# Kernel tuning notes

Measured on AMD Instinct MI355X. Metric: run time of the kernel, lower is better.

The kernel has to match this reference:

```python
import jax, jax.numpy as jnp
import numpy as np

B, S, NI, NQK, NV = 8, 2048, 1024, 128, 128

def setup_inputs() -> dict:
    key = jax.random.key(0)
    ks = jax.random.split(key, 7)
    sc_i = 1.0 / np.sqrt(NI)
    x = jax.random.normal(ks[0], (B, S, NI), dtype=jnp.float32)
    Wq = jax.random.uniform(ks[1], (NQK, NI), dtype=jnp.float32, minval=-sc_i, maxval=sc_i)
    bq = jax.random.uniform(ks[2], (NQK,), dtype=jnp.float32, minval=-sc_i, maxval=sc_i)
    Wk = jax.random.uniform(ks[3], (NQK, NI), dtype=jnp.float32, minval=-sc_i, maxval=sc_i)
    bk = jax.random.uniform(ks[4], (NQK,), dtype=jnp.float32, minval=-sc_i, maxval=sc_i)
    Wv = jax.random.uniform(ks[5], (NV, NI), dtype=jnp.float32, minval=-sc_i, maxval=sc_i)
    bv = jax.random.uniform(ks[6], (NV,), dtype=jnp.float32, minval=-sc_i, maxval=sc_i)
    return {"x": x, "Wq": Wq, "bq": bq, "Wk": Wk, "bk": bk, "Wv": Wv, "bv": bv}

def reference(x, Wq, bq, Wk, bk, Wv, bv):
    # torch nn.Linear: y = x @ W.T + b
    q = jnp.einsum('bsi,di->bsd', x, Wq) + bq  # [B,S,NQK]
    k = jnp.einsum('bsi,di->bsd', x, Wk) + bk  # [B,S,NQK]
    v = jnp.einsum('bsi,di->bsd', x, Wv) + bv  # [B,S,NV]
    # NOTE: original has no 1/sqrt(d) scaling
    Z = jnp.einsum('bqd,bkd->bqk', q, k)       # [B,S,S]
    Z = jax.nn.softmax(Z, axis=2)
    y = jnp.einsum('bqk,bkd->bqd', Z, v)       # [B,S,NV]
    return y
```

## Files before the change

kernel.cpp:

```cpp
#include <hip/hip_runtime.h>
#include <hip/hip_bf16.h>
#include <cstdint>

#define B_ 8
#define S_ 2048
#define NI_ 1024
#define D_ 128
#define M_ (B_ * S_)

typedef __attribute__((ext_vector_type(8))) short bf16x8;
typedef __attribute__((ext_vector_type(8))) unsigned short u16x8;
typedef __attribute__((ext_vector_type(4))) float f32x4;

__device__ __forceinline__ unsigned short f2bf(float f) {
    union { float f; uint32_t u; } v; v.f = f;
    uint32_t u = v.u;
    u += 0x7fff + ((u >> 16) & 1);
    return (unsigned short)(u >> 16);
}

__device__ __forceinline__ void gload16(const void* g, void* l) {
    __builtin_amdgcn_global_load_lds((const __attribute__((address_space(1))) void*)g,
                                     (__attribute__((address_space(3))) void*)l, 16, 0, 0);
}

__global__ __launch_bounds__(256) void k_cvt_x(const float* __restrict__ x,
                                               unsigned short* __restrict__ xb) {
    int t = blockIdx.x * 256 + threadIdx.x;
    long base = (long)t * 8;
    float4 a = *(const float4*)(x + base);
    float4 b = *(const float4*)(x + base + 4);
    u16x8 r;
    r[0] = f2bf(a.x); r[1] = f2bf(a.y); r[2] = f2bf(a.z); r[3] = f2bf(a.w);
    r[4] = f2bf(b.x); r[5] = f2bf(b.y); r[6] = f2bf(b.z); r[7] = f2bf(b.w);
    *(u16x8*)(xb + base) = r;
}

__global__ __launch_bounds__(256) void k_pack_w(const float* __restrict__ Wq, const float* __restrict__ bq,
                                                const float* __restrict__ Wk, const float* __restrict__ bk,
                                                const float* __restrict__ Wv, const float* __restrict__ bv,
                                                unsigned short* __restrict__ wb, float* __restrict__ bias) {
    int t = blockIdx.x * 256 + threadIdx.x;
    int e = t * 8;
    const float* src; int off;
    if (e < 131072)      { src = Wq; off = e; }
    else if (e < 262144) { src = Wk; off = e - 131072; }
    else                 { src = Wv; off = e - 262144; }
    float4 a = *(const float4*)(src + off);
    float4 b = *(const float4*)(src + off + 4);
    u16x8 r;
    r[0] = f2bf(a.x); r[1] = f2bf(a.y); r[2] = f2bf(a.z); r[3] = f2bf(a.w);
    r[4] = f2bf(b.x); r[5] = f2bf(b.y); r[6] = f2bf(b.z); r[7] = f2bf(b.w);
    *(u16x8*)(wb + e) = r;
    if (t < 384)
        bias[t] = (t < 128) ? bq[t] : (t < 256) ? bk[t - 128] : bv[t - 256];
}

__global__ __launch_bounds__(256) void k_qkv(const unsigned short* __restrict__ xb,
                                             const unsigned short* __restrict__ wb,
                                             const float* __restrict__ bias,
                                             unsigned short* __restrict__ q,
                                             unsigned short* __restrict__ kout,
                                             unsigned short* __restrict__ vT) {
    __shared__ __align__(16) unsigned short As[2][64 * 64];
    __shared__ __align__(16) unsigned short Bs[2][128 * 64];
    const int tid = threadIdx.x;
    const int m0 = blockIdx.x * 64;
    const int n0 = blockIdx.y * 128;
    const int l = tid & 63, w = tid >> 6;
    const int wr = w >> 1, wc = w & 1;
    const int lr = l & 15, lg = l >> 4;
    const int lsw = (lr & 7) << 4;

    const int srow = tid >> 3;
    const int scol = ((tid & 7) * 8) ^ (((tid >> 3) & 7) << 3);

#define GLOADA(buf, k0off) do { \
    _Pragma("unroll") \
    for (int c = 0; c < 2; c++) \
        gload16(xb + (long)(m0 + c * 32 + srow) * NI_ + (k0off) + scol, \
                (unsigned short*)As[buf] + c * 2048 + tid * 8); } while (0)

#define GLOADB(buf, k0off) do { \
    _Pragma("unroll") \
    for (int c = 0; c < 4; c++) \
        gload16(wb + (long)(n0 + c * 32 + srow) * NI_ + (k0off) + scol, \
                (unsigned short*)Bs[buf] + c * 2048 + tid * 8); } while (0)

    f32x4 acc[2][4] = {};

    GLOADA(0, 0);
    GLOADB(0, 0);
    __syncthreads();

    int cur = 0;
    for (int k0 = 0; k0 < NI_; k0 += 64) {
        bool more = (k0 + 64 < NI_);
        if (more) {
            GLOADA(cur ^ 1, k0 + 64);
            GLOADB(cur ^ 1, k0 + 64);
        }

        const char* ad = (const char*)As[cur];
        const char* bd = (const char*)Bs[cur];
        bf16x8 a[2][2], b[4][2];
#pragma unroll
        for (int i = 0; i < 2; i++)
#pragma unroll
            for (int kc = 0; kc < 2; kc++)
                a[i][kc] = *(const bf16x8*)(ad + (wr * 32 + i * 16 + lr) * 128
                                               + ((kc * 64 + lg * 16) ^ lsw));
#pragma unroll
        for (int j = 0; j < 4; j++)
#pragma unroll
            for (int kc = 0; kc < 2; kc++)
                b[j][kc] = *(const bf16x8*)(bd + (wc * 64 + j * 16 + lr) * 128
                                               + ((kc * 64 + lg * 16) ^ lsw));
#pragma unroll
        for (int kc = 0; kc < 2; kc++)
#pragma unroll
            for (int i = 0; i < 2; i++)
#pragma unroll
                for (int j = 0; j < 4; j++)
                    acc[i][j] = __builtin_amdgcn_mfma_f32_16x16x32_bf16(a[i][kc], b[j][kc], acc[i][j], 0, 0, 0);

        __syncthreads();
        cur ^= 1;
    }
#undef GLOADA
#undef GLOADB

#pragma unroll
    for (int i = 0; i < 2; i++)
#pragma unroll
        for (int j = 0; j < 4; j++)
#pragma unroll
            for (int r = 0; r < 4; r++) {
                int row = m0 + wr * 32 + i * 16 + lg * 4 + r;
                int n = n0 + wc * 64 + j * 16 + lr;
                float val = acc[i][j][r] + bias[n];
                unsigned short bv16 = f2bf(val);
                if (n0 == 0)        q[(long)row * 128 + n] = bv16;
                else if (n0 == 128) kout[(long)row * 128 + (n - 128)] = bv16;
                else {
                    int bb = row >> 11, s = row & 2047, d = n - 256;
                    vT[((long)bb * 128 + d) * (long)S_ + s] = bv16;
                }
            }
}

#define SHIFT_ 16.0f
__global__ __launch_bounds__(256, 2) void k_attn(const unsigned short* __restrict__ q,
                                                 const unsigned short* __restrict__ kk,
                                                 const unsigned short* __restrict__ vT,
                                                 float* __restrict__ o_part,
                                                 float* __restrict__ L_part) {
    __shared__ __align__(16) unsigned short Kl[2 * 64 * 128];
    __shared__ __align__(16) unsigned short Vl[2 * 128 * 64];
    __shared__ __align__(16) unsigned short Plds[4 * 32 * 64];
    const int tid = threadIdx.x, l = tid & 63, w = tid >> 6;
    const int b = blockIdx.z, ks = blockIdx.y;
    const int q0 = blockIdx.x * 128 + w * 32;
    const int lr = l & 15, lg = l >> 4;
    const unsigned short* qB = q  + (long)b * S_ * 128;
    const unsigned short* kB = kk + (long)b * S_ * 128;
    const unsigned short* vB = vT + (long)b * 128 * S_;
    char* Pw = (char*)Plds + w * 4096;
    const int kv_base = ks * 512;
    const int lsw = (lr & 7) << 4;

    const int krowc = tid >> 4;
    const int ksrc  = ((tid & 15) * 8) ^ (((tid >> 4) & 7) << 3);
    const int vrowc = tid >> 3;
    const int vsrc  = ((tid & 7) * 8) ^ (((tid >> 3) & 7) << 3);

#define STAGEKV(buf, kvoff) do { \
    unsigned short* kdst = (unsigned short*)Kl + (buf) * 8192; \
    unsigned short* vdst = (unsigned short*)Vl + (buf) * 8192; \
    _Pragma("unroll") \
    for (int c = 0; c < 4; c++) { \
        gload16(kB + (long)((kvoff) + c * 16 + krowc) * 128 + ksrc, kdst + c * 2048 + tid * 8); \
        gload16(vB + (long)(c * 32 + vrowc) * S_ + (kvoff) + vsrc,  vdst + c * 2048 + tid * 8); \
    } } while (0)

    bf16x8 qf[2][4];
#pragma unroll
    for (int a = 0; a < 2; a++)
#pragma unroll
        for (int kc = 0; kc < 4; kc++)
            qf[a][kc] = *(const bf16x8*)(qB + (long)(q0 + a * 16 + lr) * 128 + kc * 32 + lg * 8);

    STAGEKV(0, kv_base);
    __syncthreads();

    float psum[2][4] = {};
    f32x4 o[2][8] = {};
    int cur = 0;

    for (int t = 0; t < 8; t++) {
        if (t < 7) STAGEKV(cur ^ 1, kv_base + (t + 1) * 64);

        const char* kd = (const char*)Kl + cur * 16384;
        const char* vd = (const char*)Vl + cur * 16384;

        f32x4 sa[2][4] = {};
#pragma unroll
        for (int j = 0; j < 4; j++) {
            bf16x8 kf[4];
#pragma unroll
            for (int kc = 0; kc < 4; kc++)
                kf[kc] = *(const bf16x8*)(kd + (((j * 16 + lr) * 256 + kc * 64 + lg * 16) ^ lsw));
#pragma unroll
            for (int a = 0; a < 2; a++)
#pragma unroll
                for (int kc = 0; kc < 4; kc++)
                    sa[a][j] = __builtin_amdgcn_mfma_f32_16x16x32_bf16(qf[a][kc], kf[kc], sa[a][j], 0, 0, 0);
        }

#pragma unroll
        for (int a = 0; a < 2; a++)
#pragma unroll
            for (int r = 0; r < 4; r++) {
                int row = a * 16 + lg * 4 + r;
#pragma unroll
                for (int j = 0; j < 4; j++) {
                    float pj = __expf(sa[a][j][r] - SHIFT_);
                    psum[a][r] += pj;
                    int bo = (row * 128 + (j * 16 + lr) * 2) ^ ((row & 7) << 4);
                    *(unsigned short*)(Pw + bo) = f2bf(pj);
                }
            }

        bf16x8 pa[2][2];
#pragma unroll
        for (int a = 0; a < 2; a++) {
            pa[a][0] = *(const bf16x8*)(Pw + (((a * 16 + lr) * 128 + lg * 16) ^ lsw));
            pa[a][1] = *(const bf16x8*)(Pw + (((a * 16 + lr) * 128 + 64 + lg * 16) ^ lsw));
        }

#pragma unroll
        for (int c = 0; c < 8; c++) {
            int dr = c * 16 + lr;
            bf16x8 vf0 = *(const bf16x8*)(vd + ((dr * 128 + lg * 16) ^ lsw));
            bf16x8 vf1 = *(const bf16x8*)(vd + ((dr * 128 + 64 + lg * 16) ^ lsw));
#pragma unroll
            for (int a = 0; a < 2; a++) {
                o[a][c] = __builtin_amdgcn_mfma_f32_16x16x32_bf16(pa[a][0], vf0, o[a][c], 0, 0, 0);
                o[a][c] = __builtin_amdgcn_mfma_f32_16x16x32_bf16(pa[a][1], vf1, o[a][c], 0, 0, 0);
            }
        }

        __syncthreads();
        cur ^= 1;
    }
#undef STAGEKV

#pragma unroll
    for (int a = 0; a < 2; a++)
#pragma unroll
        for (int r = 0; r < 4; r++) {
            float ps = psum[a][r];
            ps += __shfl_xor(ps, 1);
            ps += __shfl_xor(ps, 2);
            ps += __shfl_xor(ps, 4);
            ps += __shfl_xor(ps, 8);
            if (lr == 0)
                L_part[((long)ks * B_ + b) * S_ + q0 + a * 16 + lg * 4 + r] = ps;
        }
#pragma unroll
    for (int a = 0; a < 2; a++)
#pragma unroll
        for (int c = 0; c < 8; c++)
#pragma unroll
            for (int r = 0; r < 4; r++) {
                int row = q0 + a * 16 + lg * 4 + r, col = c * 16 + lr;
                o_part[(((long)ks * B_ + b) * S_ + row) * 128 + col] = o[a][c][r];
            }
}

__global__ __launch_bounds__(256) void k_comb(const float* __restrict__ op,
                                              const float* __restrict__ Lp,
                                              float* __restrict__ out) {
    int t = blockIdx.x * 256 + threadIdx.x;
    int row = t >> 5;
    int c4 = (t & 31) * 4;
    float ax = 0.f, ay = 0.f, az = 0.f, aw = 0.f, Ls = 0.f;
#pragma unroll
    for (int ts = 0; ts < 4; ts++) {
        float4 v = *(const float4*)(op + (((long)ts * M_ + row) << 7) + c4);
        ax += v.x; ay += v.y; az += v.z; aw += v.w;
        Ls += Lp[(long)ts * M_ + row];
    }
    float inv = 1.f / Ls;
    float4 r; r.x = ax * inv; r.y = ay * inv; r.z = az * inv; r.w = aw * inv;
    *(float4*)(out + ((long)row << 7) + c4) = r;
}

extern "C" void kernel_launch(void* const* d_in, const int* in_sizes, int n_in,
                              void* d_out, int out_size, void* d_ws, size_t ws_size,
                              hipStream_t stream) {
    const float* x  = (const float*)d_in[0];
    const float* Wq = (const float*)d_in[1];
    const float* bq = (const float*)d_in[2];
    const float* Wk = (const float*)d_in[3];
    const float* bk = (const float*)d_in[4];
    const float* Wv = (const float*)d_in[5];
    const float* bv = (const float*)d_in[6];
    float* out = (float*)d_out;

    char* ws = (char*)d_ws;
    unsigned short* xb   = (unsigned short*)(ws);
    unsigned short* wb   = (unsigned short*)(ws + 33554432);
    float*          bias = (float*)(ws + 33554432 + 786432);
    unsigned short* qb   = (unsigned short*)(ws + 34344960);
    unsigned short* kb   = (unsigned short*)(ws + 38539264);
    unsigned short* vT   = (unsigned short*)(ws + 42733568);
    float* o_part = (float*)(ws);
    float* L_part = (float*)(ws + 46927872);

    k_cvt_x<<<8192, 256, 0, stream>>>(x, xb);
    k_pack_w<<<192, 256, 0, stream>>>(Wq, bq, Wk, bk, Wv, bv, wb, bias);
    k_qkv<<<dim3(256, 3), 256, 0, stream>>>(xb, wb, bias, qb, kb, vT);
    k_attn<<<dim3(16, 4, 8), 256, 0, stream>>>(qb, kb, vT, o_part, L_part);
    k_comb<<<2048, 256, 0, stream>>>(o_part, L_part, out);
}
```

Baseline: 81.47 us.

## Triple-buffer QKV projection GEMM with explicit vmcnt waits and raw barriers

Turns the QKV projection GEMM's double-buffered LDS pipeline into a three-stage pipeline that prefetches two K-tiles ahead. It replaces __syncthreads with explicit s_waitcnt vmcnt counts plus s_barrier and sched_barrier, so one tile's global-to-LDS loads can stay in flight during the next tile's compute. The aim is to hide more global memory latency. In exchange, LDS use per block grows by half, which may lower occupancy, and correctness now depends on hand-counted vmcnt values.

```diff
diff --git a/kernel.cpp b/kernel.cpp
--- a/kernel.cpp
+++ b/kernel.cpp
@@ -62,8 +62,8 @@
                                              unsigned short* __restrict__ q,
                                              unsigned short* __restrict__ kout,
                                              unsigned short* __restrict__ vT) {
-    __shared__ __align__(16) unsigned short As[2][64 * 64];
-    __shared__ __align__(16) unsigned short Bs[2][128 * 64];
+    __shared__ __align__(16) unsigned short As[3][64 * 64];
+    __shared__ __align__(16) unsigned short Bs[3][128 * 64];
     const int tid = threadIdx.x;
     const int m0 = blockIdx.x * 64;
     const int n0 = blockIdx.y * 128;
@@ -75,13 +75,11 @@
     const int srow = tid >> 3;
     const int scol = ((tid & 7) * 8) ^ (((tid >> 3) & 7) << 3);
 
-#define GLOADA(buf, k0off) do { \
+#define GLOADT(buf, k0off) do { \
     _Pragma("unroll") \
     for (int c = 0; c < 2; c++) \
         gload16(xb + (long)(m0 + c * 32 + srow) * NI_ + (k0off) + scol, \
-                (unsigned short*)As[buf] + c * 2048 + tid * 8); } while (0)
-
-#define GLOADB(buf, k0off) do { \
+                (unsigned short*)As[buf] + c * 2048 + tid * 8); \
     _Pragma("unroll") \
     for (int c = 0; c < 4; c++) \
         gload16(wb + (long)(n0 + c * 32 + srow) * NI_ + (k0off) + scol, \
@@ -89,27 +87,25 @@
 
     f32x4 acc[2][4] = {};
 
-    GLOADA(0, 0);
-    GLOADB(0, 0);
-    __syncthreads();
-
-    int cur = 0;
-    for (int k0 = 0; k0 < NI_; k0 += 64) {
-        bool more = (k0 + 64 < NI_);
-        if (more) {
-            GLOADA(cur ^ 1, k0 + 64);
-            GLOADB(cur ^ 1, k0 + 64);
-        }
-
-        const char* ad = (const char*)As[cur];
-        const char* bd = (const char*)Bs[cur];
+    GLOADT(0, 0);
+    GLOADT(1, 64);
+    asm volatile("s_waitcnt vmcnt(6)" ::: "memory");
+    __builtin_amdgcn_sched_barrier(0);
+    __builtin_amdgcn_s_barrier();
+    __builtin_amdgcn_sched_barrier(0);
+
+    for (int i = 0; i < 16; ++i) {
+        if (i + 2 < 16) GLOADT((i + 2) % 3, (i + 2) * 64);
+
+        const char* ad = (const char*)As + (i % 3) * 8192;
+        const char* bd = (const char*)Bs + (i % 3) * 16384;
         bf16x8 a[2][2], b[4][2];
 #pragma unroll
-        for (int i = 0; i < 2; i++)
+        for (int i2 = 0; i2 < 2; i2++)
 #pragma unroll
             for (int kc = 0; kc < 2; kc++)
-                a[i][kc] = *(const bf16x8*)(ad + (wr * 32 + i * 16 + lr) * 128
-                                               + ((kc * 64 + lg * 16) ^ lsw));
+                a[i2][kc] = *(const bf16x8*)(ad + (wr * 32 + i2 * 16 + lr) * 128
+                                                + ((kc * 64 + lg * 16) ^ lsw));
 #pragma unroll
         for (int j = 0; j < 4; j++)
 #pragma unroll
@@ -119,16 +115,20 @@
 #pragma unroll
         for (int kc = 0; kc < 2; kc++)
 #pragma unroll
-            for (int i = 0; i < 2; i++)
+            for (int i2 = 0; i2 < 2; i2++)
 #pragma unroll
                 for (int j = 0; j < 4; j++)
-                    acc[i][j] = __builtin_amdgcn_mfma_f32_16x16x32_bf16(a[i][kc], b[j][kc], acc[i][j], 0, 0, 0);
-
-        __syncthreads();
-        cur ^= 1;
+                    acc[i2][j] = __builtin_amdgcn_mfma_f32_16x16x32_bf16(a[i2][kc], b[j][kc], acc[i2][j], 0, 0, 0);
+
+        if (i < 15) {
+            if (i + 2 < 16) { asm volatile("s_waitcnt vmcnt(6)" ::: "memory"); }
+            else            { asm volatile("s_waitcnt vmcnt(0)" ::: "memory"); }
+            __builtin_amdgcn_sched_barrier(0);
+            __builtin_amdgcn_s_barrier();
+            __builtin_amdgcn_sched_barrier(0);
+        }
     }
-#undef GLOADA
-#undef GLOADB
+#undef GLOADT
 
 #pragma unroll
     for (int i = 0; i < 2; i++)
```

Result: slower. 87.61 us (+7.5%).
